# Kernel tuning notes

Measured on AMD Instinct MI355X. Metric: run time of the kernel, lower is better.

The kernel has to match this reference:

```python
import jax, jax.numpy as jnp
import numpy as np
from jax import lax

EPS = 1e-5

def index_points(points, idx):
    # points [B,N,C], idx [B,...] int -> [B,...,C]
    return jax.vmap(lambda p, i: p[i])(points, idx)

def square_distance(a, b):
    # a [B,S,3], b [B,N,3] -> [B,S,N] squared euclidean
    return (jnp.sum(a * a, -1)[:, :, None] + jnp.sum(b * b, -1)[:, None, :]
            - 2.0 * jnp.einsum('bsc,bnc->bsn', a, b))

def farthest_point_sample(xyz, npoint):
    # deterministic FPS starting at index 0 (torch version starts at a random index)
    B, N, _ = xyz.shape
    def step(carry, _):
        dist, farthest = carry
        centroid = jax.vmap(lambda p, i: p[i])(xyz, farthest)  # [B,3]
        d = jnp.sum((xyz - centroid[:, None, :]) ** 2, -1)     # [B,N]
        dist = jnp.minimum(dist, d)
        nxt = jnp.argmax(dist, -1).astype(jnp.int32)
        return (dist, nxt), farthest
    init = (jnp.full((B, N), 1e10, xyz.dtype), jnp.zeros((B,), jnp.int32))
    _, idx = lax.scan(step, init, None, length=npoint)
    return jnp.transpose(idx)  # [B, npoint]

def ball_query(radius, nsample, xyz, new_xyz):
    # replicate the torch arange/mask/sort trick: first nsample in-index-order points within radius
    B, N, _ = xyz.shape
    S = new_xyz.shape[1]
    sqrdists = square_distance(new_xyz, xyz)                      # [B,S,N]
    idx = jnp.broadcast_to(jnp.arange(N, dtype=jnp.int32), (B, S, N))
    idx = jnp.where(sqrdists > radius * radius, N, idx)
    idx = jnp.sort(idx, axis=-1)[:, :, :nsample]                  # [B,S,K]
    first = idx[:, :, :1]
    return jnp.where(idx == N, first, idx)

def conv_bn_relu(x, W, b, gamma, beta):
    # 1x1 Conv2d == per-point linear; BatchNorm2d (training mode) over (B, S, K) per channel
    h = jnp.einsum('bskc,oc->bsko', x, W) + b
    mean = jnp.mean(h, axis=(0, 1, 2))
    var = jnp.var(h, axis=(0, 1, 2))
    h = (h - mean) * (gamma / jnp.sqrt(var + EPS)) + beta
    return jax.nn.relu(h)

def set_abstraction(xyz, points, npoint, radius, nsample, W, b, gamma, beta):
    fps_idx = farthest_point_sample(xyz, npoint)                  # [B,S]
    new_xyz = index_points(xyz, fps_idx)                          # [B,S,3]
    idx = ball_query(radius, nsample, xyz, new_xyz)               # [B,S,K]
    grouped_xyz = index_points(xyz, idx) - new_xyz[:, :, None, :] # [B,S,K,3]
    if points is not None:
        new_points = jnp.concatenate([grouped_xyz, index_points(points, idx)], -1)
    else:
        new_points = grouped_xyz
    h = conv_bn_relu(new_points, W, b, gamma, beta)
    return new_xyz, jnp.max(h, axis=2)                            # [B,S,Cout]

def set_abstraction_all(xyz, points, W, b, gamma, beta):
    grouped = jnp.concatenate([xyz, points], -1)[:, None]         # [B,1,N,3+C]
    h = conv_bn_relu(grouped, W, b, gamma, beta)
    return jnp.max(h, axis=2)[:, 0]                               # [B,Cout]


def setup_inputs() -> dict:
    key = jax.random.key(0)
    ks = jax.random.split(key, 6)
    B, N, Z = 8, 8192, 256
    def lin(k, o, i):
        return jax.random.normal(k, (o, i), jnp.float32) * (1.0 / np.sqrt(i))
    f32 = jnp.float32
    return {
        'xyz': jax.random.uniform(ks[0], (B, N, 3), f32),
        'w1': lin(ks[1], 128, 3),   'b1': jnp.zeros((128,), f32),
        'g1': jnp.ones((128,), f32), 'be1': jnp.zeros((128,), f32),
        'w2': lin(ks[2], 256, 131), 'b2': jnp.zeros((256,), f32),
        'g2': jnp.ones((256,), f32), 'be2': jnp.zeros((256,), f32),
        'w3': lin(ks[3], 512, 259), 'b3': jnp.zeros((512,), f32),
        'g3': jnp.ones((512,), f32), 'be3': jnp.zeros((512,), f32),
        'wf': lin(ks[4], Z, 512),   'bf': jnp.zeros((Z,), f32),
    }


def reference(xyz, w1, b1, g1, be1, w2, b2, g2, be2, w3, b3, g3, be3, wf, bf):
    # PointNet2Encoder.forward (normal_channel=False): three set-abstraction layers + fc
    l1_xyz, l1_pts = set_abstraction(xyz, None, 512, 0.2, 32, w1, b1, g1, be1)
    l2_xyz, l2_pts = set_abstraction(l1_xyz, l1_pts, 128, 0.4, 64, w2, b2, g2, be2)
    l3 = set_abstraction_all(l2_xyz, l2_pts, w3, b3, g3, be3)     # [B,512]
    return l3 @ wf.T + bf                                         # [B, z_dim]
```

## Files before the change

### kernel.cpp

```cpp
#include <hip/hip_runtime.h>
#include <hip/hip_bf16.h>
#include <cstddef>
#include <cstdint>


__device__ __forceinline__ void fma16(float* acc, float4 a, float4 b) {
  acc[0]  = fmaf(a.x, b.x, acc[0]);
  acc[1]  = fmaf(a.x, b.y, acc[1]);
  acc[2]  = fmaf(a.x, b.z, acc[2]);
  acc[3]  = fmaf(a.x, b.w, acc[3]);
  acc[4]  = fmaf(a.y, b.x, acc[4]);
  acc[5]  = fmaf(a.y, b.y, acc[5]);
  acc[6]  = fmaf(a.y, b.z, acc[6]);
  acc[7]  = fmaf(a.y, b.w, acc[7]);
  acc[8]  = fmaf(a.z, b.x, acc[8]);
  acc[9]  = fmaf(a.z, b.y, acc[9]);
  acc[10] = fmaf(a.z, b.z, acc[10]);
  acc[11] = fmaf(a.z, b.w, acc[11]);
  acc[12] = fmaf(a.w, b.x, acc[12]);
  acc[13] = fmaf(a.w, b.y, acc[13]);
  acc[14] = fmaf(a.w, b.z, acc[14]);
  acc[15] = fmaf(a.w, b.w, acc[15]);
}

#define DPP_FMAX(v, ctrl)                                                     \
  (v) = fmaxf((v), __int_as_float(__builtin_amdgcn_update_dpp(                \
                 0, __float_as_int(v), (ctrl), 0xf, 0xf, true)))

__device__ __forceinline__ float wave_max_dpp(float v) {
  DPP_FMAX(v, 0x111);
  DPP_FMAX(v, 0x112);
  DPP_FMAX(v, 0x114);
  DPP_FMAX(v, 0x118);
  DPP_FMAX(v, 0x142);
  DPP_FMAX(v, 0x143);
  return __int_as_float(__builtin_amdgcn_readlane(__float_as_int(v), 63));
}

__device__ __forceinline__ float readlane_f(float v, int l) {
  return __int_as_float(__builtin_amdgcn_readlane(__float_as_int(v), l));
}

template<int N, int NPOINT, int TPB>
__launch_bounds__(TPB)
__global__ void fps_kernel(const float* __restrict__ xyz,
                           int* __restrict__ out_idx,
                           float* __restrict__ out_xyz) {
  constexpr int PPT = N / TPB;
  constexpr int NW = TPB / 64;
  static_assert(NW == 8, "cross-wave DPP reduce assumes 8 waves");
  __shared__ float s_wval[NW];
  __shared__ float4 s_pick;
  const int b = blockIdx.x;
  const int t = threadIdx.x;
  const int lane = t & 63;
  const int wid = t >> 6;
  const float* xb = xyz + (size_t)b * N * 3;
  float px[PPT], py[PPT], pz[PPT], dist[PPT];
#pragma unroll
  for (int j = 0; j < PPT; ++j) {
    const int n = t * PPT + j;
    px[j] = xb[n * 3 + 0];
    py[j] = xb[n * 3 + 1];
    pz[j] = xb[n * 3 + 2];
    dist[j] = 1e10f;
  }
  int far = 0;
  float cx = xb[0], cy = xb[1], cz = xb[2];
  for (int i = 0; i < NPOINT; ++i) {
    if (t == 0) {
      out_idx[b * NPOINT + i] = far;
      float* o = out_xyz + ((size_t)b * NPOINT + i) * 3;
      o[0] = cx; o[1] = cy; o[2] = cz;
    }
    float m = -1.0f;
#pragma unroll
    for (int j = 0; j < PPT; ++j) {
      const float dx = __fsub_rn(px[j], cx);
      const float dy = __fsub_rn(py[j], cy);
      const float dz = __fsub_rn(pz[j], cz);
      const float d = __fadd_rn(__fadd_rn(__fmul_rn(dx, dx), __fmul_rn(dy, dy)),
                                __fmul_rn(dz, dz));
      const float nd = fminf(dist[j], d);
      dist[j] = nd;
      m = fmaxf(m, nd);
    }
    const float wv = wave_max_dpp(m);
    if (lane == 0) s_wval[wid] = wv;
    __syncthreads();
    float x = s_wval[lane & 7];
    float y = x;
    DPP_FMAX(y, 0x111);
    DPP_FMAX(y, 0x112);
    DPP_FMAX(y, 0x114);
    const float winner =
        __int_as_float(__builtin_amdgcn_readlane(__float_as_int(y), 7));
    const unsigned long long wmask = __ballot(x == winner);
    const int first_w = __ffsll(wmask) - 1;
    if (wid == first_w) {
      const unsigned long long cand = __ballot(m == winner);
      const int fl = __ffsll(cand) - 1;
      if (lane == fl) {
        int fj = 0;
        float fx = px[0], fy = py[0], fz = pz[0];
        bool found = (dist[0] == winner);
#pragma unroll
        for (int j = 1; j < PPT; ++j) {
          const bool hit = !found && (dist[j] == winner);
          if (hit) { fj = j; fx = px[j]; fy = py[j]; fz = pz[j]; found = true; }
        }
        s_pick = make_float4(__int_as_float(t * PPT + fj), fx, fy, fz);
      }
    }
    __syncthreads();
    const float4 pk = s_pick;
    far = __float_as_int(pk.x);
    cx = pk.y; cy = pk.z; cz = pk.w;
  }
}

template<int N, int NPOINT>
__launch_bounds__(64)
__global__ void wave_fps_kernel(const float* __restrict__ xyz,
                                int* __restrict__ out_idx,
                                float* __restrict__ out_xyz) {
  constexpr int PPT = N / 64;
  const int b = blockIdx.x;
  const int lane = threadIdx.x;
  const float* xb = xyz + (size_t)b * N * 3;
  float px[PPT], py[PPT], pz[PPT], dist[PPT];
#pragma unroll
  for (int j = 0; j < PPT; ++j) {
    const int n = lane * PPT + j;
    px[j] = xb[n * 3 + 0];
    py[j] = xb[n * 3 + 1];
    pz[j] = xb[n * 3 + 2];
    dist[j] = 1e10f;
  }
  int far = 0;
  float cx = xb[0], cy = xb[1], cz = xb[2];
  for (int i = 0; i < NPOINT; ++i) {
    if (lane == 0) {
      out_idx[b * NPOINT + i] = far;
      float* o = out_xyz + ((size_t)b * NPOINT + i) * 3;
      o[0] = cx; o[1] = cy; o[2] = cz;
    }
    float m = -1.0f;
    int mj = 0;
    float mx = px[0], my = py[0], mz = pz[0];
#pragma unroll
    for (int j = 0; j < PPT; ++j) {
      const float dx = __fsub_rn(px[j], cx);
      const float dy = __fsub_rn(py[j], cy);
      const float dz = __fsub_rn(pz[j], cz);
      const float d = __fadd_rn(__fadd_rn(__fmul_rn(dx, dx), __fmul_rn(dy, dy)),
                                __fmul_rn(dz, dz));
      const float nd = fminf(dist[j], d);
      dist[j] = nd;
      const bool better = nd > m;
      m = better ? nd : m;
      mj = better ? j : mj;
      mx = better ? px[j] : mx;
      my = better ? py[j] : my;
      mz = better ? pz[j] : mz;
    }
    const float wv = wave_max_dpp(m);
    const unsigned long long cand = __ballot(m == wv);
    const int fl = __ffsll(cand) - 1;
    far = __builtin_amdgcn_readlane(lane * PPT + mj, fl);
    cx = readlane_f(mx, fl);
    cy = readlane_f(my, fl);
    cz = readlane_f(mz, fl);
  }
}

template<int N, int S, int NS>
__global__ void ballq_kernel(const float* __restrict__ xyz,
                             const float* __restrict__ new_xyz,
                             int* __restrict__ out_idx,
                             float r2) {
  const int gw = (blockIdx.x * blockDim.x + threadIdx.x) >> 6;
  const int lane = threadIdx.x & 63;
  if (gw >= 8 * S) return;
  const int b = gw / S;
  const int s = gw % S;
  const float* c = new_xyz + ((size_t)b * S + s) * 3;
  const float cx = c[0], cy = c[1], cz = c[2];
  const float sa = __fadd_rn(__fadd_rn(__fmul_rn(cx, cx), __fmul_rn(cy, cy)),
                             __fmul_rn(cz, cz));
  const float* xb = xyz + (size_t)b * N * 3;
  int* out = out_idx + ((size_t)b * S + s) * NS;
  int cnt = 0;
  int first = -1;
  for (int n0 = 0; n0 < N && cnt < NS; n0 += 64) {
    const int n = n0 + lane;
    const float x = xb[n * 3 + 0];
    const float y = xb[n * 3 + 1];
    const float z = xb[n * 3 + 2];
    const float sb = __fadd_rn(__fadd_rn(__fmul_rn(x, x), __fmul_rn(y, y)),
                               __fmul_rn(z, z));
    const float dt = __fadd_rn(__fadd_rn(__fmul_rn(x, cx), __fmul_rn(y, cy)),
                               __fmul_rn(z, cz));
    const float d = __fsub_rn(__fadd_rn(sa, sb), __fmul_rn(2.0f, dt));
    const bool in = !(d > r2);
    const unsigned long long m = __ballot(in);
    if (in) {
      const int pos = cnt + __popcll(m & ((1ull << lane) - 1ull));
      if (pos < NS) out[pos] = n;
    }
    if (first < 0 && m) first = n0 + __ffsll((unsigned long long)m) - 1;
    cnt += __popcll(m);
  }
  for (int j = cnt + lane; j < NS; j += 64) out[j] = first;
}

__global__ void mom1_kernel(const float* __restrict__ xyz,
                            const float* __restrict__ l1_xyz,
                            const int* __restrict__ idx1,
                            float* __restrict__ part) {
  const int t = threadIdx.x;
  const int r = blockIdx.x * 256 + t;
  const int bs = r >> 5;
  const int b = r >> 14;
  const int idx = idx1[r];
  const float* p = xyz + ((size_t)(b << 13) + idx) * 3;
  const float* q = l1_xyz + (size_t)bs * 3;
  const float x = p[0] - q[0];
  const float y = p[1] - q[1];
  const float z = p[2] - q[2];
  float vals[9] = {x, y, z, x * x, x * y, x * z, y * y, y * z, z * z};
  __shared__ float sw[4][9];
  const int lane = t & 63, wid = t >> 6;
#pragma unroll
  for (int v = 0; v < 9; ++v) {
    float a = vals[v];
#pragma unroll
    for (int off = 32; off; off >>= 1) a += __shfl_xor(a, off);
    if (lane == 0) sw[wid][v] = a;
  }
  __syncthreads();
  if (t == 0) {
#pragma unroll
    for (int v = 0; v < 9; ++v)
      part[blockIdx.x * 12 + v] = sw[0][v] + sw[1][v] + sw[2][v] + sw[3][v];
  }
}

__global__ void stats1_kernel(const float* __restrict__ part,
                              const float* __restrict__ w1,
                              const float* __restrict__ b1,
                              const float* __restrict__ g1,
                              const float* __restrict__ be1,
                              float* __restrict__ ss1) {
  __shared__ double sm[9];
  const int t = threadIdx.x;
  if (t < 9) {
    double a = 0.0;
    for (int k = 0; k < 512; ++k) a += (double)part[k * 12 + t];
    sm[t] = a;
  }
  __syncthreads();
  const double n = 131072.0;
  const double mu0 = sm[0] / n, mu1 = sm[1] / n, mu2 = sm[2] / n;
  const double C00 = sm[3] / n - mu0 * mu0;
  const double C01 = sm[4] / n - mu0 * mu1;
  const double C02 = sm[5] / n - mu0 * mu2;
  const double C11 = sm[6] / n - mu1 * mu1;
  const double C12 = sm[7] / n - mu1 * mu2;
  const double C22 = sm[8] / n - mu2 * mu2;
  if (t < 128) {
    const double w0 = w1[t * 3], w1_ = w1[t * 3 + 1], w2 = w1[t * 3 + 2];
    const double mh = w0 * mu0 + w1_ * mu1 + w2 * mu2 + (double)b1[t];
    const double var = w0 * w0 * C00 + w1_ * w1_ * C11 + w2 * w2 * C22 +
                       2.0 * (w0 * w1_ * C01 + w0 * w2 * C02 + w1_ * w2 * C12);
    const float scale = g1[t] / sqrtf((float)var + 1e-5f);
    const float shift = be1[t] - (float)mh * scale;
    ss1[t * 2] = scale;
    ss1[t * 2 + 1] = shift;
  }
}

__global__ void conv1max_kernel(const float* __restrict__ xyz,
                                const float* __restrict__ l1_xyz,
                                const int* __restrict__ idx1,
                                const float* __restrict__ w1,
                                const float* __restrict__ b1,
                                const float* __restrict__ ss1,
                                float* __restrict__ l1_pts) {
  const int bs = blockIdx.x;
  const int b = bs >> 9;
  const int t = threadIdx.x;
  __shared__ float sx[32][3];
  if (t < 32) {
    const int idx = idx1[bs * 32 + t];
    const float* p = xyz + ((size_t)(b << 13) + idx) * 3;
    const float* q = l1_xyz + (size_t)bs * 3;
    sx[t][0] = p[0] - q[0];
    sx[t][1] = p[1] - q[1];
    sx[t][2] = p[2] - q[2];
  }
  __syncthreads();
  const float w0 = w1[t * 3], wa = w1[t * 3 + 1], wb = w1[t * 3 + 2];
  const float bo = b1[t];
  float hmax = -1e30f, hmin = 1e30f;
#pragma unroll 8
  for (int k = 0; k < 32; ++k) {
    const float h = sx[k][0] * w0 + sx[k][1] * wa + sx[k][2] * wb + bo;
    hmax = fmaxf(hmax, h);
    hmin = fminf(hmin, h);
  }
  const float scale = ss1[t * 2], shift = ss1[t * 2 + 1];
  const float hsel = (scale >= 0.f) ? hmax : hmin;
  l1_pts[(size_t)bs * 128 + t] = fmaxf(hsel * scale + shift, 0.0f);
}

#define MOM2_BLOCKS 256
#define MOM2_S2 (132 * 132)
#define MOM2_STRIDE (MOM2_S2 + 132)

__global__ __launch_bounds__(256)
void mom2_kernel(const float* __restrict__ l1_xyz,
                 const float* __restrict__ l1_pts,
                 const float* __restrict__ l2_xyz,
                 const int* __restrict__ idx2,
                 float* __restrict__ part) {
  __shared__ __align__(16) float xs[64 * 132];
  const int t = threadIdx.x;
  const int blk = blockIdx.x;
  float acc[5][16];
#pragma unroll
  for (int tt = 0; tt < 5; ++tt)
#pragma unroll
    for (int j = 0; j < 16; ++j) acc[tt][j] = 0.f;
  float s1 = 0.f;
  const int rbase = blk * 256;
  for (int sb = 0; sb < 4; ++sb) {
    __syncthreads();
    for (int e = t; e < 64 * 131; e += 256) {
      const int rr = e / 131, cc = e % 131;
      const int r = rbase + sb * 64 + rr;
      const int b = r >> 13;
      const int s = (r >> 6) & 127;
      const int idx = idx2[r];
      float v;
      if (cc < 3)
        v = l1_xyz[((size_t)(b << 9) + idx) * 3 + cc] -
            l2_xyz[((size_t)(b << 7) + s) * 3 + cc];
      else
        v = l1_pts[((size_t)(b << 9) + idx) * 128 + (cc - 3)];
      xs[rr * 132 + cc] = v;
    }
    if (t < 64) xs[t * 132 + 131] = 0.f;
    __syncthreads();
#pragma unroll
    for (int tt = 0; tt < 5; ++tt) {
      const int tile = t + tt * 256;
      if (tile < 33 * 33) {
        const int i0 = (tile % 33) * 4;
        const int j0 = (tile / 33) * 4;
        for (int r = 0; r < 64; ++r) {
          const float4 a = *(const float4*)&xs[r * 132 + i0];
          const float4 bb = *(const float4*)&xs[r * 132 + j0];
          fma16(acc[tt], a, bb);
        }
      }
    }
    if (t < 132) {
      for (int r = 0; r < 64; ++r) s1 += xs[r * 132 + t];
    }
  }
  float* pb = part + (size_t)blk * MOM2_STRIDE;
#pragma unroll
  for (int tt = 0; tt < 5; ++tt) {
    const int tile = t + tt * 256;
    if (tile < 33 * 33) {
      const int i0 = (tile % 33) * 4;
      const int j0 = (tile / 33) * 4;
#pragma unroll
      for (int ii = 0; ii < 4; ++ii)
#pragma unroll
        for (int jj = 0; jj < 4; ++jj)
          pb[(i0 + ii) * 132 + (j0 + jj)] = acc[tt][ii * 4 + jj];
    }
  }
  if (t < 132) pb[MOM2_S2 + t] = s1;
}

__global__ void reduce2_kernel(const float* __restrict__ part,
                               double* __restrict__ out) {
  const int e = blockIdx.x * 256 + threadIdx.x;
  if (e >= MOM2_STRIDE) return;
  double a = 0.0;
  for (int k = 0; k < MOM2_BLOCKS; ++k)
    a += (double)part[(size_t)k * MOM2_STRIDE + e];
  out[e] = a;
}

__global__ void stats2_kernel(const double* __restrict__ mom,
                              const float* __restrict__ w2,
                              const float* __restrict__ b2,
                              const float* __restrict__ g2,
                              const float* __restrict__ be2,
                              float* __restrict__ ss2) {
  const int o = blockIdx.x;
  const int t = threadIdx.x;
  const float* w = w2 + o * 131;
  double q = 0.0, md = 0.0;
  for (int i = t; i < 131; i += 128) {
    const double wi = (double)w[i];
    double di = 0.0;
    for (int j = 0; j < 131; ++j) di += mom[i * 132 + j] * (double)w[j];
    q += wi * di;
    md += wi * mom[MOM2_S2 + i];
  }
  __shared__ double sq[128], smd[128];
  sq[t] = q;
  smd[t] = md;
  __syncthreads();
  for (int off = 64; off; off >>= 1) {
    if (t < off) { sq[t] += sq[t + off]; smd[t] += smd[t + off]; }
    __syncthreads();
  }
  if (t == 0) {
    const double n = 65536.0;
    const double mdot = smd[0] / n;
    const double var = sq[0] / n - mdot * mdot;
    const double mean = mdot + (double)b2[o];
    const float scale = g2[o] / sqrtf((float)var + 1e-5f);
    const float shift = be2[o] - (float)mean * scale;
    ss2[o * 2] = scale;
    ss2[o * 2 + 1] = shift;
  }
}

__global__ __launch_bounds__(128)
void conv2max_kernel(const float* __restrict__ l1_xyz,
                     const float* __restrict__ l1_pts,
                     const float* __restrict__ l2_xyz,
                     const int* __restrict__ idx2,
                     const float* __restrict__ w2,
                     const float* __restrict__ b2,
                     const float* __restrict__ ss2,
                     float* __restrict__ l2_pts) {
  __shared__ __align__(16) float xT[131 * 68];
  __shared__ __align__(16) float wT[131 * 36];
  __shared__ float red[16 * 32];
  const int bs = blockIdx.x;
  const int b = bs >> 7;
  const int t = threadIdx.x;
  for (int e = t; e < 64 * 131; e += 128) {
    const int k = e / 131, cc = e % 131;
    const int idx = idx2[bs * 64 + k];
    float v;
    if (cc < 3)
      v = l1_xyz[((size_t)(b << 9) + idx) * 3 + cc] - l2_xyz[(size_t)bs * 3 + cc];
    else
      v = l1_pts[((size_t)(b << 9) + idx) * 128 + (cc - 3)];
    xT[cc * 68 + k] = v;
  }
  const int ty = t >> 3;
  const int tx = t & 7;
  for (int oc = 0; oc < 8; ++oc) {
    __syncthreads();
    for (int e = t; e < 32 * 131; e += 128) {
      const int oo = e / 131, cc = e % 131;
      wT[cc * 36 + oo] = w2[(oc * 32 + oo) * 131 + cc];
    }
    __syncthreads();
    float acc[16];
#pragma unroll
    for (int j = 0; j < 16; ++j) acc[j] = 0.f;
    for (int c = 0; c < 131; ++c) {
      const float4 a = *(const float4*)&xT[c * 68 + ty * 4];
      const float4 w4 = *(const float4*)&wT[c * 36 + tx * 4];
      fma16(acc, a, w4);
    }
#pragma unroll
    for (int oo = 0; oo < 4; ++oo) {
      const int o = oc * 32 + tx * 4 + oo;
      const float bo = b2[o];
      const float hmax = fmaxf(fmaxf(acc[0 + oo], acc[4 + oo]),
                               fmaxf(acc[8 + oo], acc[12 + oo])) + bo;
      const float hmin = fminf(fminf(acc[0 + oo], acc[4 + oo]),
                               fminf(acc[8 + oo], acc[12 + oo])) + bo;
      const float scale = ss2[o * 2], shift = ss2[o * 2 + 1];
      const float hsel = (scale >= 0.f) ? hmax : hmin;
      red[ty * 32 + tx * 4 + oo] = fmaxf(hsel * scale + shift, 0.f);
    }
    __syncthreads();
    if (t < 32) {
      float m = red[t];
#pragma unroll
      for (int w = 1; w < 16; ++w) m = fmaxf(m, red[w * 32 + t]);
      l2_pts[(size_t)bs * 256 + oc * 32 + t] = m;
    }
  }
}

__global__ __launch_bounds__(256)
void conv3_kernel(const float* __restrict__ l2_xyz,
                  const float* __restrict__ l2_pts,
                  const float* __restrict__ w3,
                  const float* __restrict__ b3,
                  float* __restrict__ h3T) {
  __shared__ __align__(16) float aT[96 * 68];
  __shared__ __align__(16) float wT[96 * 68];
  const int t = threadIdx.x;
  const int r0 = (blockIdx.x & 15) * 64;
  const int o0 = (blockIdx.x >> 4) * 64;
  const int ty = t >> 4, tx = t & 15;
  float acc[16];
#pragma unroll
  for (int j = 0; j < 16; ++j) acc[j] = 0.f;
  for (int c0 = 0; c0 < 259; c0 += 96) {
    __syncthreads();
    for (int e = t; e < 96 * 64; e += 256) {
      const int rr = e / 96, cc = e - rr * 96;
      const int c = c0 + cc;
      const int r = r0 + rr;
      float v = 0.f;
      if (c < 259)
        v = (c < 3) ? l2_xyz[(size_t)r * 3 + c]
                    : l2_pts[(size_t)r * 256 + (c - 3)];
      aT[cc * 68 + rr] = v;
    }
    for (int e = t; e < 96 * 64; e += 256) {
      const int oo = e / 96, cc = e - oo * 96;
      const int c = c0 + cc;
      wT[cc * 68 + oo] = (c < 259) ? w3[(size_t)(o0 + oo) * 259 + c] : 0.f;
    }
    __syncthreads();
    for (int cc = 0; cc < 96; ++cc) {
      const float4 a = *(const float4*)&aT[cc * 68 + ty * 4];
      const float4 w4 = *(const float4*)&wT[cc * 68 + tx * 4];
      fma16(acc, a, w4);
    }
  }
#pragma unroll
  for (int kk = 0; kk < 4; ++kk)
#pragma unroll
    for (int oo = 0; oo < 4; ++oo) {
      const int o = o0 + tx * 4 + oo;
      const int r = r0 + ty * 4 + kk;
      h3T[(size_t)o * 1024 + r] = acc[kk * 4 + oo] + b3[o];
    }
}

__global__ void bn3max_kernel(const float* __restrict__ h3T,
                              const float* __restrict__ g3,
                              const float* __restrict__ be3,
                              float* __restrict__ l3) {
  const int o = blockIdx.x;
  const int t = threadIdx.x;
  const float4 v = *(const float4*)&h3T[(size_t)o * 1024 + t * 4];
  double s = (double)v.x + (double)v.y + (double)v.z + (double)v.w;
  double s2 = (double)v.x * v.x + (double)v.y * v.y + (double)v.z * v.z +
              (double)v.w * v.w;
  __shared__ double sa_[256], sb_[256];
  sa_[t] = s;
  sb_[t] = s2;
  __syncthreads();
  for (int off = 128; off; off >>= 1) {
    if (t < off) { sa_[t] += sa_[t + off]; sb_[t] += sb_[t + off]; }
    __syncthreads();
  }
  const double mean = sa_[0] / 1024.0;
  const double var = sb_[0] / 1024.0 - mean * mean;
  const float scale = g3[o] / sqrtf((float)var + 1e-5f);
  const float shift = be3[o] - (float)mean * scale;
  const float hmax = fmaxf(fmaxf(v.x, v.y), fmaxf(v.z, v.w));
  const float hmin = fminf(fminf(v.x, v.y), fminf(v.z, v.w));
  const float hsel = (scale >= 0.f) ? hmax : hmin;
  __shared__ float rm[256];
  rm[t] = fmaxf(hsel * scale + shift, 0.f);
  __syncthreads();
  if (t < 8) {
    float m = rm[t * 32];
#pragma unroll
    for (int j = 1; j < 32; ++j) m = fmaxf(m, rm[t * 32 + j]);
    l3[t * 512 + o] = m;
  }
}

__global__ void final_kernel(const float* __restrict__ l3,
                             const float* __restrict__ wf,
                             const float* __restrict__ bf,
                             float* __restrict__ out) {
  const int b = blockIdx.x;
  const int t = threadIdx.x;
  __shared__ float s[512];
  s[t] = l3[b * 512 + t];
  s[t + 256] = l3[b * 512 + t + 256];
  __syncthreads();
  float acc = bf[t];
  for (int o = 0; o < 512; ++o) acc = fmaf(wf[(size_t)t * 512 + o], s[o], acc);
  out[b * 256 + t] = acc;
}

extern "C" void kernel_launch(void* const* d_in, const int* in_sizes, int n_in,
                              void* d_out, int out_size, void* d_ws, size_t ws_size,
                              hipStream_t stream) {
  (void)in_sizes; (void)n_in; (void)out_size; (void)ws_size;
  const float* xyz = (const float*)d_in[0];
  const float* w1 = (const float*)d_in[1];
  const float* b1 = (const float*)d_in[2];
  const float* g1 = (const float*)d_in[3];
  const float* be1 = (const float*)d_in[4];
  const float* w2 = (const float*)d_in[5];
  const float* b2 = (const float*)d_in[6];
  const float* g2 = (const float*)d_in[7];
  const float* be2 = (const float*)d_in[8];
  const float* w3 = (const float*)d_in[9];
  const float* b3 = (const float*)d_in[10];
  const float* g3 = (const float*)d_in[11];
  const float* be3 = (const float*)d_in[12];
  const float* wf = (const float*)d_in[13];
  const float* bf = (const float*)d_in[14];
  float* out = (float*)d_out;

  char* base = (char*)d_ws;
  size_t off = 0;
  auto alloc = [&](size_t bytes) -> char* {
    off = (off + 511) & ~(size_t)511;
    char* p = base + off;
    off += bytes;
    return p;
  };
  int* fps1_idx = (int*)alloc(8 * 512 * 4);
  float* l1_xyz = (float*)alloc(8 * 512 * 3 * 4);
  int* idx1 = (int*)alloc((size_t)8 * 512 * 32 * 4);
  float* part1 = (float*)alloc(512 * 12 * 4);
  float* ss1 = (float*)alloc(128 * 2 * 4);
  float* l1_pts = (float*)alloc((size_t)8 * 512 * 128 * 4);
  int* fps2_idx = (int*)alloc(8 * 128 * 4);
  float* l2_xyz = (float*)alloc(8 * 128 * 3 * 4);
  int* idx2 = (int*)alloc((size_t)8 * 128 * 64 * 4);
  float* part2 = (float*)alloc((size_t)MOM2_BLOCKS * MOM2_STRIDE * 4);
  double* mom2d = (double*)alloc((size_t)MOM2_STRIDE * 8);
  float* ss2 = (float*)alloc(256 * 2 * 4);
  float* l2_pts = (float*)alloc((size_t)8 * 128 * 256 * 4);
  float* h3T = (float*)alloc((size_t)512 * 1024 * 4);
  float* l3 = (float*)alloc(8 * 512 * 4);

  const float r2_1 = (float)(0.2 * 0.2);
  const float r2_2 = (float)(0.4 * 0.4);

  fps_kernel<8192, 512, 512><<<8, 512, 0, stream>>>(xyz, fps1_idx, l1_xyz);
  ballq_kernel<8192, 512, 32><<<1024, 256, 0, stream>>>(xyz, l1_xyz, idx1, r2_1);
  mom1_kernel<<<512, 256, 0, stream>>>(xyz, l1_xyz, idx1, part1);
  stats1_kernel<<<1, 128, 0, stream>>>(part1, w1, b1, g1, be1, ss1);
  conv1max_kernel<<<4096, 128, 0, stream>>>(xyz, l1_xyz, idx1, w1, b1, ss1, l1_pts);
  wave_fps_kernel<512, 128><<<8, 64, 0, stream>>>(l1_xyz, fps2_idx, l2_xyz);
  ballq_kernel<512, 128, 64><<<256, 256, 0, stream>>>(l1_xyz, l2_xyz, idx2, r2_2);
  mom2_kernel<<<MOM2_BLOCKS, 256, 0, stream>>>(l1_xyz, l1_pts, l2_xyz, idx2, part2);
  reduce2_kernel<<<(MOM2_STRIDE + 255) / 256, 256, 0, stream>>>(part2, mom2d);
  stats2_kernel<<<256, 128, 0, stream>>>(mom2d, w2, b2, g2, be2, ss2);
  conv2max_kernel<<<1024, 128, 0, stream>>>(l1_xyz, l1_pts, l2_xyz, idx2, w2, b2,
                                            ss2, l2_pts);
  conv3_kernel<<<128, 256, 0, stream>>>(l2_xyz, l2_pts, w3, b3, h3T);
  bn3max_kernel<<<512, 256, 0, stream>>>(h3T, g3, be3, l3);
  final_kernel<<<8, 256, 0, stream>>>(l3, wf, bf, out);
}
```

Before: 1.235 ms.

## Buffer FPS picks in LDS, exploit Gram symmetry, retile conv2max over all outputs

The FPS kernel now records each selected index and coordinate in a shared-memory history and writes all outputs at the end, so thread 0 no longer issues global stores inside the serial loop. The second-moment kernel computes only the upper triangle of the 132x132 Gram matrix using 8x8 register tiles and mirrors the result on store, roughly halving the FMA work. conv2max is rewritten to use 256 threads that compute all 256 output channels at once over input-channel chunks, and it defers the BN scale/shift to a final max/min reduction. In exchange it uses more registers per thread (64 accumulators) and the symmetric tiling leaves some threads idle.

After: 1.123 ms (median of 2 runs). 1.1x faster.

```diff
diff --git a/kernel.cpp b/kernel.cpp
--- a/kernel.cpp
+++ b/kernel.cpp
@@ -50,7 +50,7 @@
   constexpr int NW = TPB / 64;
   static_assert(NW == 8, "cross-wave DPP reduce assumes 8 waves");
   __shared__ float s_wval[NW];
-  __shared__ float4 s_pick;
+  __shared__ __align__(16) float4 s_hist[NPOINT];
   const int b = blockIdx.x;
   const int t = threadIdx.x;
   const int lane = t & 63;
@@ -65,14 +65,9 @@
     pz[j] = xb[n * 3 + 2];
     dist[j] = 1e10f;
   }
-  int far = 0;
   float cx = xb[0], cy = xb[1], cz = xb[2];
-  for (int i = 0; i < NPOINT; ++i) {
-    if (t == 0) {
-      out_idx[b * NPOINT + i] = far;
-      float* o = out_xyz + ((size_t)b * NPOINT + i) * 3;
-      o[0] = cx; o[1] = cy; o[2] = cz;
-    }
+  if (t == 0) s_hist[0] = make_float4(__int_as_float(0), cx, cy, cz);
+  for (int i = 0; i < NPOINT - 1; ++i) {
     float m = -1.0f;
 #pragma unroll
     for (int j = 0; j < PPT; ++j) {
@@ -109,13 +104,18 @@
           const bool hit = !found && (dist[j] == winner);
           if (hit) { fj = j; fx = px[j]; fy = py[j]; fz = pz[j]; found = true; }
         }
-        s_pick = make_float4(__int_as_float(t * PPT + fj), fx, fy, fz);
+        s_hist[i + 1] = make_float4(__int_as_float(t * PPT + fj), fx, fy, fz);
       }
     }
     __syncthreads();
-    const float4 pk = s_pick;
-    far = __float_as_int(pk.x);
+    const float4 pk = s_hist[i + 1];
     cx = pk.y; cy = pk.z; cz = pk.w;
+  }
+  for (int e = t; e < NPOINT; e += TPB) {
+    const float4 h = s_hist[e];
+    out_idx[b * NPOINT + e] = __float_as_int(h.x);
+    float* o = out_xyz + ((size_t)b * NPOINT + e) * 3;
+    o[0] = h.y; o[1] = h.z; o[2] = h.w;
   }
 }
 
@@ -324,63 +324,74 @@
                  const float* __restrict__ l2_xyz,
                  const int* __restrict__ idx2,
                  float* __restrict__ part) {
-  __shared__ __align__(16) float xs[64 * 132];
+  __shared__ __align__(16) float xs[64 * 136];
   const int t = threadIdx.x;
   const int blk = blockIdx.x;
-  float acc[5][16];
-#pragma unroll
-  for (int tt = 0; tt < 5; ++tt)
-#pragma unroll
-    for (int j = 0; j < 16; ++j) acc[tt][j] = 0.f;
+  int ti = -1, tj = 0;
+  {
+    int u = t;
+    for (int r = 0; r < 17; ++r) {
+      const int cnt = 17 - r;
+      if (u < cnt) { ti = r; tj = r + u; break; }
+      u -= cnt;
+    }
+  }
+  const bool active = (ti >= 0);
+  float acc[64];
+#pragma unroll
+  for (int j = 0; j < 64; ++j) acc[j] = 0.f;
   float s1 = 0.f;
   const int rbase = blk * 256;
   for (int sb = 0; sb < 4; ++sb) {
     __syncthreads();
-    for (int e = t; e < 64 * 131; e += 256) {
-      const int rr = e / 131, cc = e % 131;
+    for (int e = t; e < 64 * 136; e += 256) {
+      const int rr = e / 136, cc = e % 136;
       const int r = rbase + sb * 64 + rr;
       const int b = r >> 13;
       const int s = (r >> 6) & 127;
       const int idx = idx2[r];
-      float v;
+      float v = 0.f;
       if (cc < 3)
         v = l1_xyz[((size_t)(b << 9) + idx) * 3 + cc] -
             l2_xyz[((size_t)(b << 7) + s) * 3 + cc];
-      else
+      else if (cc < 131)
         v = l1_pts[((size_t)(b << 9) + idx) * 128 + (cc - 3)];
-      xs[rr * 132 + cc] = v;
-    }
-    if (t < 64) xs[t * 132 + 131] = 0.f;
-    __syncthreads();
-#pragma unroll
-    for (int tt = 0; tt < 5; ++tt) {
-      const int tile = t + tt * 256;
-      if (tile < 33 * 33) {
-        const int i0 = (tile % 33) * 4;
-        const int j0 = (tile / 33) * 4;
-        for (int r = 0; r < 64; ++r) {
-          const float4 a = *(const float4*)&xs[r * 132 + i0];
-          const float4 bb = *(const float4*)&xs[r * 132 + j0];
-          fma16(acc[tt], a, bb);
+      xs[rr * 136 + cc] = v;
+    }
+    __syncthreads();
+    if (active) {
+      for (int r = 0; r < 64; ++r) {
+        const float4 a0 = *(const float4*)&xs[r * 136 + ti * 8];
+        const float4 a1 = *(const float4*)&xs[r * 136 + ti * 8 + 4];
+        const float4 b0 = *(const float4*)&xs[r * 136 + tj * 8];
+        const float4 b1 = *(const float4*)&xs[r * 136 + tj * 8 + 4];
+        fma16(acc + 0,  a0, b0);
+        fma16(acc + 16, a0, b1);
+        fma16(acc + 32, a1, b0);
+        fma16(acc + 48, a1, b1);
+      }
+    }
+    if (t < 132) {
+      for (int r = 0; r < 64; ++r) s1 += xs[r * 136 + t];
+    }
+  }
+  float* pb = part + (size_t)blk * MOM2_STRIDE;
+  if (active) {
+#pragma unroll
+    for (int ii = 0; ii < 8; ++ii) {
+      const int gi = ti * 8 + ii;
+      if (gi < 132) {
+#pragma unroll
+        for (int jj = 0; jj < 8; ++jj) {
+          const int gj = tj * 8 + jj;
+          if (gj < 132) {
+            const float v =
+                acc[(ii >> 2) * 32 + (jj >> 2) * 16 + (ii & 3) * 4 + (jj & 3)];
+            pb[gi * 132 + gj] = v;
+            if (ti != tj) pb[gj * 132 + gi] = v;
+          }
         }
       }
-    }
-    if (t < 132) {
-      for (int r = 0; r < 64; ++r) s1 += xs[r * 132 + t];
-    }
-  }
-  float* pb = part + (size_t)blk * MOM2_STRIDE;
-#pragma unroll
-  for (int tt = 0; tt < 5; ++tt) {
-    const int tile = t + tt * 256;
-    if (tile < 33 * 33) {
-      const int i0 = (tile % 33) * 4;
-      const int j0 = (tile / 33) * 4;
-#pragma unroll
-      for (int ii = 0; ii < 4; ++ii)
-#pragma unroll
-        for (int jj = 0; jj < 4; ++jj)
-          pb[(i0 + ii) * 132 + (j0 + jj)] = acc[tt][ii * 4 + jj];
     }
   }
   if (t < 132) pb[MOM2_S2 + t] = s1;
@@ -433,7 +444,7 @@
   }
 }
 
-__global__ __launch_bounds__(128)
+__global__ __launch_bounds__(256)
 void conv2max_kernel(const float* __restrict__ l1_xyz,
                      const float* __restrict__ l1_pts,
                      const float* __restrict__ l2_xyz,
@@ -442,58 +453,88 @@
                      const float* __restrict__ b2,
                      const float* __restrict__ ss2,
                      float* __restrict__ l2_pts) {
-  __shared__ __align__(16) float xT[131 * 68];
-  __shared__ __align__(16) float wT[131 * 36];
-  __shared__ float red[16 * 32];
+  __shared__ __align__(16) float xT[33 * 68];
+  __shared__ __align__(16) float wT[33 * 260];
+  __shared__ float redmax[8 * 256];
+  __shared__ float redmin[8 * 256];
   const int bs = blockIdx.x;
   const int b = bs >> 7;
   const int t = threadIdx.x;
-  for (int e = t; e < 64 * 131; e += 128) {
-    const int k = e / 131, cc = e % 131;
-    const int idx = idx2[bs * 64 + k];
-    float v;
-    if (cc < 3)
-      v = l1_xyz[((size_t)(b << 9) + idx) * 3 + cc] - l2_xyz[(size_t)bs * 3 + cc];
-    else
-      v = l1_pts[((size_t)(b << 9) + idx) * 128 + (cc - 3)];
-    xT[cc * 68 + k] = v;
-  }
-  const int ty = t >> 3;
-  const int tx = t & 7;
-  for (int oc = 0; oc < 8; ++oc) {
-    __syncthreads();
-    for (int e = t; e < 32 * 131; e += 128) {
-      const int oo = e / 131, cc = e % 131;
-      wT[cc * 36 + oo] = w2[(oc * 32 + oo) * 131 + cc];
-    }
-    __syncthreads();
-    float acc[16];
-#pragma unroll
-    for (int j = 0; j < 16; ++j) acc[j] = 0.f;
-    for (int c = 0; c < 131; ++c) {
-      const float4 a = *(const float4*)&xT[c * 68 + ty * 4];
-      const float4 w4 = *(const float4*)&wT[c * 36 + tx * 4];
-      fma16(acc, a, w4);
-    }
-#pragma unroll
-    for (int oo = 0; oo < 4; ++oo) {
-      const int o = oc * 32 + tx * 4 + oo;
-      const float bo = b2[o];
-      const float hmax = fmaxf(fmaxf(acc[0 + oo], acc[4 + oo]),
-                               fmaxf(acc[8 + oo], acc[12 + oo])) + bo;
-      const float hmin = fminf(fminf(acc[0 + oo], acc[4 + oo]),
-                               fminf(acc[8 + oo], acc[12 + oo])) + bo;
-      const float scale = ss2[o * 2], shift = ss2[o * 2 + 1];
-      const float hsel = (scale >= 0.f) ? hmax : hmin;
-      red[ty * 32 + tx * 4 + oo] = fmaxf(hsel * scale + shift, 0.f);
-    }
-    __syncthreads();
-    if (t < 32) {
-      float m = red[t];
-#pragma unroll
-      for (int w = 1; w < 16; ++w) m = fmaxf(m, red[w * 32 + t]);
-      l2_pts[(size_t)bs * 256 + oc * 32 + t] = m;
-    }
+  const int ty = t >> 5;
+  const int tx = t & 31;
+  float acc[64];
+#pragma unroll
+  for (int j = 0; j < 64; ++j) acc[j] = 0.f;
+  for (int ch = 0; ch < 4; ++ch) {
+    const int c0 = ch * 33;
+    const int CC = (ch == 3) ? 32 : 33;
+    __syncthreads();
+    for (int e = t; e < 64 * CC; e += 256) {
+      const int k = e / CC, cc = e % CC;
+      const int idx = idx2[bs * 64 + k];
+      const int c = c0 + cc;
+      float v;
+      if (c < 3)
+        v = l1_xyz[((size_t)(b << 9) + idx) * 3 + c] -
+            l2_xyz[(size_t)bs * 3 + c];
+      else
+        v = l1_pts[((size_t)(b << 9) + idx) * 128 + (c - 3)];
+      xT[cc * 68 + k] = v;
+    }
+    for (int e = t; e < 256 * CC; e += 256) {
+      const int oo = e / CC, cc = e % CC;
+      wT[cc * 260 + oo] = w2[oo * 131 + c0 + cc];
+    }
+    __syncthreads();
+    for (int cc = 0; cc < CC; ++cc) {
+      const float4 a0 = *(const float4*)&xT[cc * 68 + ty * 8];
+      const float4 a1 = *(const float4*)&xT[cc * 68 + ty * 8 + 4];
+      const float4 w0 = *(const float4*)&wT[cc * 260 + tx * 4];
+      const float4 w1 = *(const float4*)&wT[cc * 260 + 128 + tx * 4];
+      fma16(acc + 0,  a0, w0);
+      fma16(acc + 16, a0, w1);
+      fma16(acc + 32, a1, w0);
+      fma16(acc + 48, a1, w1);
+    }
+  }
+#pragma unroll
+  for (int bi = 0; bi < 4; ++bi) {
+    float mxA = acc[bi], mnA = acc[bi];
+    float mxB = acc[16 + bi], mnB = acc[16 + bi];
+#pragma unroll
+    for (int ai = 1; ai < 4; ++ai) {
+      mxA = fmaxf(mxA, acc[ai * 4 + bi]);
+      mnA = fminf(mnA, acc[ai * 4 + bi]);
+      mxB = fmaxf(mxB, acc[16 + ai * 4 + bi]);
+      mnB = fminf(mnB, acc[16 + ai * 4 + bi]);
+    }
+#pragma unroll
+    for (int ai = 0; ai < 4; ++ai) {
+      mxA = fmaxf(mxA, acc[32 + ai * 4 + bi]);
+      mnA = fminf(mnA, acc[32 + ai * 4 + bi]);
+      mxB = fmaxf(mxB, acc[48 + ai * 4 + bi]);
+      mnB = fminf(mnB, acc[48 + ai * 4 + bi]);
+    }
+    redmax[ty * 256 + tx * 4 + bi] = mxA;
+    redmin[ty * 256 + tx * 4 + bi] = mnA;
+    redmax[ty * 256 + 128 + tx * 4 + bi] = mxB;
+    redmin[ty * 256 + 128 + tx * 4 + bi] = mnB;
+  }
+  __syncthreads();
+  {
+    const int o = t;
+    float mx = redmax[o], mn = redmin[o];
+#pragma unroll
+    for (int w = 1; w < 8; ++w) {
+      mx = fmaxf(mx, redmax[w * 256 + o]);
+      mn = fminf(mn, redmin[w * 256 + o]);
+    }
+    const float bo = b2[o];
+    const float hmax = mx + bo;
+    const float hmin = mn + bo;
+    const float scale = ss2[o * 2], shift = ss2[o * 2 + 1];
+    const float hsel = (scale >= 0.f) ? hmax : hmin;
+    l2_pts[(size_t)bs * 256 + o] = fmaxf(hsel * scale + shift, 0.f);
   }
 }
 
@@ -655,7 +696,7 @@
   mom2_kernel<<<MOM2_BLOCKS, 256, 0, stream>>>(l1_xyz, l1_pts, l2_xyz, idx2, part2);
   reduce2_kernel<<<(MOM2_STRIDE + 255) / 256, 256, 0, stream>>>(part2, mom2d);
   stats2_kernel<<<256, 128, 0, stream>>>(mom2d, w2, b2, g2, be2, ss2);
-  conv2max_kernel<<<1024, 128, 0, stream>>>(l1_xyz, l1_pts, l2_xyz, idx2, w2, b2,
+  conv2max_kernel<<<1024, 256, 0, stream>>>(l1_xyz, l1_pts, l2_xyz, idx2, w2, b2,
                                             ss2, l2_pts);
   conv3_kernel<<<128, 256, 0, stream>>>(l2_xyz, l2_pts, w3, b3, h3T);
   bn3max_kernel<<<512, 256, 0, stream>>>(h3T, g3, be3, l3);
```
